# Kernel tuning notes

Hardware: AMD Instinct MI355X
Metric: run time of the kernel (lower is better)

The kernel has to match this reference:

```python
import jax, jax.numpy as jnp
import numpy as np

NEG_BIG = -9e15
LRELU_SLOPE = 0.2  # alpha

N = 8192
IN_F = 256
OUT_F = 128


def setup_inputs() -> dict:
    key = jax.random.key(0)
    k1, k2, k3, k4 = jax.random.split(key, 4)
    inputs = jax.random.normal(k1, (N, IN_F), dtype=jnp.float32)
    adj = jax.random.randint(k2, (N, N), 0, 2, dtype=jnp.int32)
    # xavier_uniform with gain=1.414
    gain = 1.414
    bW = gain * np.sqrt(6.0 / (IN_F + OUT_F))
    W = jax.random.uniform(k3, (IN_F, OUT_F), minval=-bW, maxval=bW, dtype=jnp.float32)
    ba = gain * np.sqrt(6.0 / (2 * OUT_F + 1))
    a = jax.random.uniform(k4, (2 * OUT_F, 1), minval=-ba, maxval=ba, dtype=jnp.float32)
    return {"inputs": inputs, "adj": adj, "W": W, "a": a}


def reference(inputs, adj, W, a):
    # h: [N, F']
    h = inputs @ W
    # a^T [h_i || h_j] = h_i . a[:F'] + h_j . a[F':]  -- avoids the O(N^2 * 2F') concat
    a1 = a[:OUT_F, 0]   # [F']
    a2 = a[OUT_F:, 0]   # [F']
    s1 = h @ a1         # [N]
    s2 = h @ a2         # [N]
    e = s1[:, None] + s2[None, :]                      # [N, N]
    e = jnp.where(e >= 0, e, LRELU_SLOPE * e)          # LeakyReLU(alpha)
    scores = jnp.where(adj > 0, e, jnp.float32(NEG_BIG))
    attention = jax.nn.softmax(scores, axis=1)         # row softmax; dropout p=0
    h_prime = attention @ h                            # [N, F']
    return jax.nn.elu(h_prime)                         # concat=True -> elu
```

## Files before the change

kernel.cpp:

```cpp
#include <hip/hip_runtime.h>
#include <hip/hip_bf16.h>

#define NN   8192
#define INF_ 256
#define OUTF 128
#define SLOPE 0.2f

typedef float f32x4  __attribute__((ext_vector_type(4)));
typedef float f32x16 __attribute__((ext_vector_type(16)));
typedef short bf16x8 __attribute__((ext_vector_type(8)));
typedef int   i32x4  __attribute__((ext_vector_type(4)));
typedef unsigned short u16;
typedef u16 u16x4 __attribute__((ext_vector_type(4)));

__device__ __forceinline__ u16 f2bf(float f) {
  return __builtin_bit_cast(u16, __float2bfloat16(f));
}

__global__ __launch_bounds__(256) void gat_k1(
    const float* __restrict__ X, const float* __restrict__ W,
    const float* __restrict__ a, u16* __restrict__ hbF,
    float* __restrict__ s1, float* __restrict__ s2) {
  __shared__ float xs[32 * INF_];
  const int t = threadIdx.x;
  const int r0 = blockIdx.x * 32;
  {
    const f32x4* src = (const f32x4*)(X + (size_t)r0 * INF_);
    f32x4* dst = (f32x4*)xs;
    for (int i = t; i < 32 * INF_ / 4; i += 256) dst[i] = src[i];
  }
  __syncthreads();
  const int cg = t & 31;
  const int rg = t >> 5;
  float acc[4][4];
#pragma unroll
  for (int i = 0; i < 4; i++)
#pragma unroll
    for (int j = 0; j < 4; j++) acc[i][j] = 0.f;

  for (int k = 0; k < INF_; k += 4) {
    f32x4 xv[4];
#pragma unroll
    for (int i = 0; i < 4; i++) xv[i] = *(const f32x4*)&xs[(rg * 4 + i) * INF_ + k];
#pragma unroll
    for (int kk = 0; kk < 4; kk++) {
      f32x4 wv = *(const f32x4*)&W[(k + kk) * OUTF + cg * 4];
#pragma unroll
      for (int i = 0; i < 4; i++)
#pragma unroll
        for (int j = 0; j < 4; j++) acc[i][j] = fmaf(xv[i][kk], wv[j], acc[i][j]);
    }
  }

  f32x4 a1v = *(const f32x4*)&a[cg * 4];
  f32x4 a2v = *(const f32x4*)&a[OUTF + cg * 4];
  float p1[4], p2[4];
#pragma unroll
  for (int i = 0; i < 4; i++) {
    p1[i] = acc[i][0] * a1v[0] + acc[i][1] * a1v[1] + acc[i][2] * a1v[2] + acc[i][3] * a1v[3];
    p2[i] = acc[i][0] * a2v[0] + acc[i][1] * a2v[1] + acc[i][2] * a2v[2] + acc[i][3] * a2v[3];
  }
#pragma unroll
  for (int m = 1; m < 32; m <<= 1) {
#pragma unroll
    for (int i = 0; i < 4; i++) {
      p1[i] += __shfl_xor(p1[i], m);
      p2[i] += __shfl_xor(p2[i], m);
    }
  }
  if (cg == 0) {
#pragma unroll
    for (int i = 0; i < 4; i++) {
      s1[r0 + rg * 4 + i] = p1[i];
      s2[r0 + rg * 4 + i] = p2[i];
    }
  }

  const int R0 = r0 + rg * 4;
  const int J  = R0 >> 4;
  const int gg = (R0 >> 3) & 1;
  const int e0 = R0 & 7;
#pragma unroll
  for (int j = 0; j < 4; j++) {
    const int C = cg * 4 + j;
    u16x4 pk;
#pragma unroll
    for (int i = 0; i < 4; i++) pk[i] = f2bf(acc[i][j]);
    size_t flat = ((size_t)(J * 4 + (C >> 5)) * 64 + (C & 31) + 32 * gg) * 8 + e0;
    *(u16x4*)(hbF + flat) = pk;
  }
}

__global__ __launch_bounds__(256) void gat_k2(const float* __restrict__ s2,
                                              float* __restrict__ s2m) {
  __shared__ float sm[4];
  const int t = threadIdx.x;
  float m = -1e30f;
  for (int i = t; i < NN; i += 256) m = fmaxf(m, s2[i]);
#pragma unroll
  for (int k = 1; k < 64; k <<= 1) m = fmaxf(m, __shfl_xor(m, k));
  if ((t & 63) == 0) sm[t >> 6] = m;
  __syncthreads();
  if (t == 0) *s2m = fmaxf(fmaxf(sm[0], sm[1]), fmaxf(sm[2], sm[3]));
}

__device__ __forceinline__ void st16(float* dst, const f32x16& A, int g) {
#pragma unroll
  for (int r = 0; r < 16; r++) {
    const int dr = (r & 3) + 8 * (r >> 2) + 4 * g;
    dst[dr * 128] = A[r];
  }
}
__device__ __forceinline__ void ad16(float* dst, const f32x16& A, int g) {
#pragma unroll
  for (int r = 0; r < 16; r++) {
    const int dr = (r & 3) + 8 * (r >> 2) + 4 * g;
    dst[dr * 128] += A[r];
  }
}

__global__ __launch_bounds__(512, 2) void gat_k3(
    const int* __restrict__ adj, const u16* __restrict__ hbF,
    const float* __restrict__ s1g, const float* __restrict__ s2g,
    const float* __restrict__ s2maxp, float* __restrict__ out) {
  __shared__ float lred[4 * 32 * 128];
  const int t = threadIdx.x;
  const int w = t >> 6;
  const int l = t & 63;
  const int r0 = blockIdx.x * 32;
  const int row = l & 31;
  const int g = l >> 5;

  const float s1r = s1g[r0 + row];
  const float s2m = *s2maxp;
  float Mi = s1r + s2m;
  Mi = fmaxf(Mi, SLOPE * Mi);

  f32x16 acc0 = 0.f, acc1 = 0.f, acc2 = 0.f, acc3 = 0.f;

  const i32x4* adjp = (const i32x4*)(adj + (size_t)(r0 + row) * NN + 8 * g);
  const f32x4* s2p  = (const f32x4*)(s2g + 8 * g);
  const bf16x8* bp  = (const bf16x8*)hbF;

  i32x4 a0c = adjp[4 * w], a1c = adjp[4 * w + 1];
  f32x4 s0c = s2p[4 * w],  s1c = s2p[4 * w + 1];
  bf16x8 b0c = bp[(size_t)(w * 4 + 0) * 64 + l];
  bf16x8 b1c = bp[(size_t)(w * 4 + 1) * 64 + l];
  bf16x8 b2c = bp[(size_t)(w * 4 + 2) * 64 + l];
  bf16x8 b3c = bp[(size_t)(w * 4 + 3) * 64 + l];

  float dsum = 0.f;
  for (int n = w; n < 512; n += 8) {
    const int nn = (n + 8 < 512) ? (n + 8) : w;
    i32x4 a0n = adjp[4 * nn], a1n = adjp[4 * nn + 1];
    f32x4 s0n = s2p[4 * nn],  s1n = s2p[4 * nn + 1];
    bf16x8 b0n = bp[(size_t)(nn * 4 + 0) * 64 + l];
    bf16x8 b1n = bp[(size_t)(nn * 4 + 1) * 64 + l];
    bf16x8 b2n = bp[(size_t)(nn * 4 + 2) * 64 + l];
    bf16x8 b3n = bp[(size_t)(nn * 4 + 3) * 64 + l];

    bf16x8 af;
#pragma unroll
    for (int e = 0; e < 8; e++) {
      float x = s1r + ((e < 4) ? s0c[e] : s1c[e - 4]);
      x = fmaxf(x, SLOPE * x);
      float p = __expf(x - Mi);
      const int ad = (e < 4) ? a0c[e] : a1c[e - 4];
      p = (ad > 0) ? p : 0.f;
      dsum += p;
      af[e] = (short)f2bf(p);
    }
    acc0 = __builtin_amdgcn_mfma_f32_32x32x16_bf16(af, b0c, acc0, 0, 0, 0);
    acc1 = __builtin_amdgcn_mfma_f32_32x32x16_bf16(af, b1c, acc1, 0, 0, 0);
    acc2 = __builtin_amdgcn_mfma_f32_32x32x16_bf16(af, b2c, acc2, 0, 0, 0);
    acc3 = __builtin_amdgcn_mfma_f32_32x32x16_bf16(af, b3c, acc3, 0, 0, 0);

    a0c = a0n; a1c = a1n; s0c = s0n; s1c = s1n;
    b0c = b0n; b1c = b1n; b2c = b2n; b3c = b3n;
  }

  dsum += __shfl_xor(dsum, 32);
  if (l < 32) lred[w * 32 + l] = dsum;
  __syncthreads();
  if (t < 32) {
    float d = 0.f;
#pragma unroll
    for (int w8 = 0; w8 < 8; w8++) d += lred[w8 * 32 + t];
    lred[256 + t] = d;
  }
  __syncthreads();
  const float myden = fmaxf(lred[256 + (t >> 4)], 1e-30f);
  __syncthreads();

  const int colw = l & 31;
  if (w < 4) {
    st16(&lred[w * 4096 + 0 * 32 + colw], acc0, g);
    st16(&lred[w * 4096 + 1 * 32 + colw], acc1, g);
    st16(&lred[w * 4096 + 2 * 32 + colw], acc2, g);
    st16(&lred[w * 4096 + 3 * 32 + colw], acc3, g);
  }
  __syncthreads();
  if (w >= 4) {
    ad16(&lred[(w - 4) * 4096 + 0 * 32 + colw], acc0, g);
    ad16(&lred[(w - 4) * 4096 + 1 * 32 + colw], acc1, g);
    ad16(&lred[(w - 4) * 4096 + 2 * 32 + colw], acc2, g);
    ad16(&lred[(w - 4) * 4096 + 3 * 32 + colw], acc3, g);
  }
  __syncthreads();

  const int orow = t >> 4;
  const int oc = (t & 15) * 8;
  float o[8];
#pragma unroll
  for (int i = 0; i < 8; i++) o[i] = 0.f;
#pragma unroll
  for (int b = 0; b < 4; b++)
#pragma unroll
    for (int i = 0; i < 8; i++) o[i] += lred[b * 4096 + orow * 128 + oc + i];

  float res[8];
#pragma unroll
  for (int i = 0; i < 8; i++) {
    float v = o[i] / myden;
    res[i] = (v > 0.f) ? v : expm1f(v);
  }
  float* op = out + (size_t)(r0 + orow) * OUTF + oc;
  *(f32x4*)op = (f32x4){res[0], res[1], res[2], res[3]};
  *(f32x4*)(op + 4) = (f32x4){res[4], res[5], res[6], res[7]};
}

extern "C" void kernel_launch(void* const* d_in, const int* in_sizes, int n_in,
                              void* d_out, int out_size, void* d_ws, size_t ws_size,
                              hipStream_t stream) {
  (void)in_sizes; (void)n_in; (void)out_size; (void)ws_size;
  const float* X  = (const float*)d_in[0];
  const int*  adj = (const int*)d_in[1];
  const float* W  = (const float*)d_in[2];
  const float* a  = (const float*)d_in[3];
  float* out = (float*)d_out;

  u16*   hbF = (u16*)d_ws;
  float* s1  = (float*)((char*)d_ws + (size_t)2 * 1024 * 1024);
  float* s2  = s1 + NN;
  float* s2m = s2 + NN;

  gat_k1<<<NN / 32, 256, 0, stream>>>(X, W, a, hbF, s1, s2);
  gat_k2<<<1, 256, 0, stream>>>(s2, s2m);
  gat_k3<<<NN / 32, 512, 0, stream>>>(adj, hbF, s1, s2, s2m, out);
}
```

Before: 117.2 us.

## Stage adjacency tiles through double-buffered swizzled LDS with coalesced loads

```diff
diff --git a/kernel.cpp b/kernel.cpp
--- a/kernel.cpp
+++ b/kernel.cpp
@@ -123,7 +123,7 @@
     const int* __restrict__ adj, const u16* __restrict__ hbF,
     const float* __restrict__ s1g, const float* __restrict__ s2g,
     const float* __restrict__ s2maxp, float* __restrict__ out) {
-  __shared__ float lred[4 * 32 * 128];
+  __shared__ int adjs[2 * 32 * 256];
   const int t = threadIdx.x;
   const int w = t >> 6;
   const int l = t & 63;
@@ -138,46 +138,83 @@
 
   f32x16 acc0 = 0.f, acc1 = 0.f, acc2 = 0.f, acc3 = 0.f;
 
-  const i32x4* adjp = (const i32x4*)(adj + (size_t)(r0 + row) * NN + 8 * g);
-  const f32x4* s2p  = (const f32x4*)(s2g + 8 * g);
-  const bf16x8* bp  = (const bf16x8*)hbF;
-
-  i32x4 a0c = adjp[4 * w], a1c = adjp[4 * w + 1];
-  f32x4 s0c = s2p[4 * w],  s1c = s2p[4 * w + 1];
-  bf16x8 b0c = bp[(size_t)(w * 4 + 0) * 64 + l];
-  bf16x8 b1c = bp[(size_t)(w * 4 + 1) * 64 + l];
-  bf16x8 b2c = bp[(size_t)(w * 4 + 2) * 64 + l];
-  bf16x8 b3c = bp[(size_t)(w * 4 + 3) * 64 + l];
-
+  const int srow = t >> 4;
+  const int sc4 = (t & 15) * 4;
+  const int* gsrc = adj + (size_t)(r0 + srow) * NN + sc4;
+  const int swz_s = (srow & 7) << 2;
+  const int swz_r = (row & 7) << 2;
+
+  i32x4 st[4];
+#define STAGE_LOAD(TL)                                         \
+  {                                                            \
+    const int* p_ = gsrc + 256 * (TL);                         \
+    st[0] = *(const i32x4*)(p_);                               \
+    st[1] = *(const i32x4*)(p_ + 64);                          \
+    st[2] = *(const i32x4*)(p_ + 128);                         \
+    st[3] = *(const i32x4*)(p_ + 192);                         \
+  }
+#define STAGE_WRITE(BUF)                                                    \
+  {                                                                         \
+    int* b_ = &adjs[(BUF) * 8192 + srow * 256];                             \
+    *(i32x4*)(b_ + ((sc4 + 0) ^ swz_s))   = st[0];                          \
+    *(i32x4*)(b_ + ((sc4 + 64) ^ swz_s))  = st[1];                          \
+    *(i32x4*)(b_ + ((sc4 + 128) ^ swz_s)) = st[2];                          \
+    *(i32x4*)(b_ + ((sc4 + 192) ^ swz_s)) = st[3];                          \
+  }
+
+  const bf16x8* bp = (const bf16x8*)hbF;
   float dsum = 0.f;
-  for (int n = w; n < 512; n += 8) {
-    const int nn = (n + 8 < 512) ? (n + 8) : w;
-    i32x4 a0n = adjp[4 * nn], a1n = adjp[4 * nn + 1];
-    f32x4 s0n = s2p[4 * nn],  s1n = s2p[4 * nn + 1];
-    bf16x8 b0n = bp[(size_t)(nn * 4 + 0) * 64 + l];
-    bf16x8 b1n = bp[(size_t)(nn * 4 + 1) * 64 + l];
-    bf16x8 b2n = bp[(size_t)(nn * 4 + 2) * 64 + l];
-    bf16x8 b3n = bp[(size_t)(nn * 4 + 3) * 64 + l];
-
-    bf16x8 af;
-#pragma unroll
-    for (int e = 0; e < 8; e++) {
-      float x = s1r + ((e < 4) ? s0c[e] : s1c[e - 4]);
-      x = fmaxf(x, SLOPE * x);
-      float p = __expf(x - Mi);
-      const int ad = (e < 4) ? a0c[e] : a1c[e - 4];
-      p = (ad > 0) ? p : 0.f;
-      dsum += p;
-      af[e] = (short)f2bf(p);
-    }
-    acc0 = __builtin_amdgcn_mfma_f32_32x32x16_bf16(af, b0c, acc0, 0, 0, 0);
-    acc1 = __builtin_amdgcn_mfma_f32_32x32x16_bf16(af, b1c, acc1, 0, 0, 0);
-    acc2 = __builtin_amdgcn_mfma_f32_32x32x16_bf16(af, b2c, acc2, 0, 0, 0);
-    acc3 = __builtin_amdgcn_mfma_f32_32x32x16_bf16(af, b3c, acc3, 0, 0, 0);
-
-    a0c = a0n; a1c = a1n; s0c = s0n; s1c = s1n;
-    b0c = b0n; b1c = b1n; b2c = b2n; b3c = b3n;
-  }
+
+  STAGE_LOAD(0);
+  STAGE_WRITE(0);
+  STAGE_LOAD(1);
+  __syncthreads();
+
+  int cur = 0;
+  for (int tt = 0; tt < 32; tt++) {
+    bf16x8 b[8];
+    const int n0 = 16 * tt + w;
+#pragma unroll
+    for (int k = 0; k < 2; k++) {
+      const int n = n0 + 8 * k;
+#pragma unroll
+      for (int q = 0; q < 4; q++)
+        b[k * 4 + q] = bp[(size_t)(n * 4 + q) * 64 + l];
+    }
+
+    const int* abuf = &adjs[cur * 8192 + row * 256];
+#pragma unroll
+    for (int k = 0; k < 2; k++) {
+      const int jj0 = 128 * k + 16 * w + 8 * g;
+      i32x4 A0 = *(const i32x4*)(abuf + ((jj0) ^ swz_r));
+      i32x4 A1 = *(const i32x4*)(abuf + ((jj0 + 4) ^ swz_r));
+      const int j0 = 256 * tt + jj0;
+      f32x4 s0 = *(const f32x4*)(s2g + j0);
+      f32x4 s1v = *(const f32x4*)(s2g + j0 + 4);
+      bf16x8 af;
+#pragma unroll
+      for (int e = 0; e < 8; e++) {
+        float x = s1r + ((e < 4) ? s0[e] : s1v[e - 4]);
+        x = fmaxf(x, SLOPE * x);
+        float p = __expf(x - Mi);
+        const int ad = (e < 4) ? A0[e] : A1[e - 4];
+        p = (ad > 0) ? p : 0.f;
+        dsum += p;
+        af[e] = (short)f2bf(p);
+      }
+      acc0 = __builtin_amdgcn_mfma_f32_32x32x16_bf16(af, b[k * 4 + 0], acc0, 0, 0, 0);
+      acc1 = __builtin_amdgcn_mfma_f32_32x32x16_bf16(af, b[k * 4 + 1], acc1, 0, 0, 0);
+      acc2 = __builtin_amdgcn_mfma_f32_32x32x16_bf16(af, b[k * 4 + 2], acc2, 0, 0, 0);
+      acc3 = __builtin_amdgcn_mfma_f32_32x32x16_bf16(af, b[k * 4 + 3], acc3, 0, 0, 0);
+    }
+
+    STAGE_WRITE(cur ^ 1);
+    STAGE_LOAD(tt + 2 < 32 ? tt + 2 : 0);
+    __syncthreads();
+    cur ^= 1;
+  }
+
+  float* lred = (float*)adjs;
 
   dsum += __shfl_xor(dsum, 32);
   if (l < 32) lred[w * 32 + l] = dsum;
@@ -214,9 +251,9 @@
 #pragma unroll
   for (int i = 0; i < 8; i++) o[i] = 0.f;
 #pragma unroll
-  for (int b = 0; b < 4; b++)
-#pragma unroll
-    for (int i = 0; i < 8; i++) o[i] += lred[b * 4096 + orow * 128 + oc + i];
+  for (int bq = 0; bq < 4; bq++)
+#pragma unroll
+    for (int i = 0; i < 8; i++) o[i] += lred[bq * 4096 + orow * 128 + oc + i];
 
   float res[8];
 #pragma unroll
```

Measured after the change: 116.6 us. No clear change (-0.5%).

## Split attention columns across blocks, stage adj tiles in LDS, add reduction kernel

Applied to the files above, without the earlier changes.

```diff
diff --git a/kernel.cpp b/kernel.cpp
--- a/kernel.cpp
+++ b/kernel.cpp
@@ -5,6 +5,9 @@
 #define INF_ 256
 #define OUTF 128
 #define SLOPE 0.2f
+#define NJC  4
+#define JCHUNK (NN / NJC)
+#define NT   (JCHUNK / 128)
 
 typedef float f32x4  __attribute__((ext_vector_type(4)));
 typedef float f32x16 __attribute__((ext_vector_type(16)));
@@ -119,15 +122,20 @@
   }
 }
 
-__global__ __launch_bounds__(512, 2) void gat_k3(
+__global__ __launch_bounds__(512, 4) void gat_k3(
     const int* __restrict__ adj, const u16* __restrict__ hbF,
     const float* __restrict__ s1g, const float* __restrict__ s2g,
-    const float* __restrict__ s2maxp, float* __restrict__ out) {
-  __shared__ float lred[4 * 32 * 128];
+    const float* __restrict__ s2maxp, float* __restrict__ part,
+    float* __restrict__ dpart) {
+  __shared__ int adjs[2 * 4096];
+  __shared__ float dred[256];
   const int t = threadIdx.x;
   const int w = t >> 6;
   const int l = t & 63;
-  const int r0 = blockIdx.x * 32;
+  const int rb = blockIdx.x & 255;
+  const int jc = blockIdx.x >> 8;
+  const int r0 = rb * 32;
+  const int j0 = jc * JCHUNK;
   const int row = l & 31;
   const int g = l >> 5;
 
@@ -138,95 +146,146 @@
 
   f32x16 acc0 = 0.f, acc1 = 0.f, acc2 = 0.f, acc3 = 0.f;
 
-  const i32x4* adjp = (const i32x4*)(adj + (size_t)(r0 + row) * NN + 8 * g);
-  const f32x4* s2p  = (const f32x4*)(s2g + 8 * g);
-  const bf16x8* bp  = (const bf16x8*)hbF;
-
-  i32x4 a0c = adjp[4 * w], a1c = adjp[4 * w + 1];
-  f32x4 s0c = s2p[4 * w],  s1c = s2p[4 * w + 1];
-  bf16x8 b0c = bp[(size_t)(w * 4 + 0) * 64 + l];
-  bf16x8 b1c = bp[(size_t)(w * 4 + 1) * 64 + l];
-  bf16x8 b2c = bp[(size_t)(w * 4 + 2) * 64 + l];
-  bf16x8 b3c = bp[(size_t)(w * 4 + 3) * 64 + l];
-
+  const int srow = t >> 4;
+  const int scg = t & 15;
+  const int cA = 4 * scg + ((srow & 1) ? 64 : 0);
+  const int cB = 4 * scg + ((srow & 1) ? 0 : 64);
+  const int slotA = ((cA >> 2) ^ srow) & 31;
+  const int slotB = ((cB >> 2) ^ srow) & 31;
+  const int* gsrc = adj + (size_t)(r0 + srow) * NN + j0;
+
+  i32x4 stA, stB;
+#define STAGE_LOAD(TL)                              \
+  {                                                 \
+    const int* p_ = gsrc + 128 * (TL);              \
+    stA = *(const i32x4*)(p_ + cA);                 \
+    stB = *(const i32x4*)(p_ + cB);                 \
+  }
+#define STAGE_WRITE(BUF)                            \
+  {                                                 \
+    int* b_ = &adjs[(BUF) * 4096 + srow * 128];     \
+    *(i32x4*)(b_ + slotA * 4) = stA;                \
+    *(i32x4*)(b_ + slotB * 4) = stB;                \
+  }
+
+  const int c0 = 16 * w + 8 * g;
+  const int sl0 = (((c0 >> 2) + 0) ^ row) & 31;
+  const int sl1 = (((c0 >> 2) + 1) ^ row) & 31;
+
+  const bf16x8* bp = (const bf16x8*)hbF;
+  const float* s2b = s2g + j0;
   float dsum = 0.f;
-  for (int n = w; n < 512; n += 8) {
-    const int nn = (n + 8 < 512) ? (n + 8) : w;
-    i32x4 a0n = adjp[4 * nn], a1n = adjp[4 * nn + 1];
-    f32x4 s0n = s2p[4 * nn],  s1n = s2p[4 * nn + 1];
-    bf16x8 b0n = bp[(size_t)(nn * 4 + 0) * 64 + l];
-    bf16x8 b1n = bp[(size_t)(nn * 4 + 1) * 64 + l];
-    bf16x8 b2n = bp[(size_t)(nn * 4 + 2) * 64 + l];
-    bf16x8 b3n = bp[(size_t)(nn * 4 + 3) * 64 + l];
+
+  STAGE_LOAD(0);
+  STAGE_WRITE(0);
+  STAGE_LOAD(1);
+  __syncthreads();
+
+  int cur = 0;
+  for (int tt = 0; tt < NT; tt++) {
+    const int n = jc * 128 + 8 * tt + w;
+    const bf16x8* bq = bp + (size_t)(n * 4) * 64 + l;
+    bf16x8 b0 = bq[0], b1 = bq[64], b2 = bq[128], b3 = bq[192];
+
+    const int* abuf = &adjs[cur * 4096 + row * 128];
+    i32x4 A0 = *(const i32x4*)(abuf + sl0 * 4);
+    i32x4 A1 = *(const i32x4*)(abuf + sl1 * 4);
+    f32x4 s0  = *(const f32x4*)(s2b + 128 * tt + c0);
+    f32x4 s1v = *(const f32x4*)(s2b + 128 * tt + c0 + 4);
 
     bf16x8 af;
 #pragma unroll
     for (int e = 0; e < 8; e++) {
-      float x = s1r + ((e < 4) ? s0c[e] : s1c[e - 4]);
+      float x = s1r + ((e < 4) ? s0[e] : s1v[e - 4]);
       x = fmaxf(x, SLOPE * x);
       float p = __expf(x - Mi);
-      const int ad = (e < 4) ? a0c[e] : a1c[e - 4];
+      const int ad = (e < 4) ? A0[e] : A1[e - 4];
       p = (ad > 0) ? p : 0.f;
       dsum += p;
       af[e] = (short)f2bf(p);
     }
-    acc0 = __builtin_amdgcn_mfma_f32_32x32x16_bf16(af, b0c, acc0, 0, 0, 0);
-    acc1 = __builtin_amdgcn_mfma_f32_32x32x16_bf16(af, b1c, acc1, 0, 0, 0);
-    acc2 = __builtin_amdgcn_mfma_f32_32x32x16_bf16(af, b2c, acc2, 0, 0, 0);
-    acc3 = __builtin_amdgcn_mfma_f32_32x32x16_bf16(af, b3c, acc3, 0, 0, 0);
-
-    a0c = a0n; a1c = a1n; s0c = s0n; s1c = s1n;
-    b0c = b0n; b1c = b1n; b2c = b2n; b3c = b3n;
+    acc0 = __builtin_amdgcn_mfma_f32_32x32x16_bf16(af, b0, acc0, 0, 0, 0);
+    acc1 = __builtin_amdgcn_mfma_f32_32x32x16_bf16(af, b1, acc1, 0, 0, 0);
+    acc2 = __builtin_amdgcn_mfma_f32_32x32x16_bf16(af, b2, acc2, 0, 0, 0);
+    acc3 = __builtin_amdgcn_mfma_f32_32x32x16_bf16(af, b3, acc3, 0, 0, 0);
+
+    if (tt + 1 < NT) STAGE_WRITE(cur ^ 1);
+    if (tt + 2 < NT) STAGE_LOAD(tt + 2);
+    __syncthreads();
+    cur ^= 1;
   }
 
   dsum += __shfl_xor(dsum, 32);
-  if (l < 32) lred[w * 32 + l] = dsum;
-  __syncthreads();
-  if (t < 32) {
-    float d = 0.f;
-#pragma unroll
-    for (int w8 = 0; w8 < 8; w8++) d += lred[w8 * 32 + t];
-    lred[256 + t] = d;
-  }
-  __syncthreads();
-  const float myden = fmaxf(lred[256 + (t >> 4)], 1e-30f);
-  __syncthreads();
-
+  if (l < 32) dred[w * 32 + l] = dsum;
+
+  float* lred = (float*)adjs;
   const int colw = l & 31;
-  if (w < 4) {
+  if (w < 2) {
     st16(&lred[w * 4096 + 0 * 32 + colw], acc0, g);
     st16(&lred[w * 4096 + 1 * 32 + colw], acc1, g);
     st16(&lred[w * 4096 + 2 * 32 + colw], acc2, g);
     st16(&lred[w * 4096 + 3 * 32 + colw], acc3, g);
   }
   __syncthreads();
-  if (w >= 4) {
+  if (t < 32) {
+    float d = 0.f;
+#pragma unroll
+    for (int w8 = 0; w8 < 8; w8++) d += dred[w8 * 32 + t];
+    dpart[jc * NN + r0 + t] = d;
+  }
+  if (w == 2 || w == 3) {
+    ad16(&lred[(w - 2) * 4096 + 0 * 32 + colw], acc0, g);
+    ad16(&lred[(w - 2) * 4096 + 1 * 32 + colw], acc1, g);
+    ad16(&lred[(w - 2) * 4096 + 2 * 32 + colw], acc2, g);
+    ad16(&lred[(w - 2) * 4096 + 3 * 32 + colw], acc3, g);
+  }
+  __syncthreads();
+  if (w == 4 || w == 5) {
     ad16(&lred[(w - 4) * 4096 + 0 * 32 + colw], acc0, g);
     ad16(&lred[(w - 4) * 4096 + 1 * 32 + colw], acc1, g);
     ad16(&lred[(w - 4) * 4096 + 2 * 32 + colw], acc2, g);
     ad16(&lred[(w - 4) * 4096 + 3 * 32 + colw], acc3, g);
   }
   __syncthreads();
-
-  const int orow = t >> 4;
-  const int oc = (t & 15) * 8;
-  float o[8];
-#pragma unroll
-  for (int i = 0; i < 8; i++) o[i] = 0.f;
-#pragma unroll
-  for (int b = 0; b < 4; b++)
-#pragma unroll
-    for (int i = 0; i < 8; i++) o[i] += lred[b * 4096 + orow * 128 + oc + i];
-
-  float res[8];
-#pragma unroll
-  for (int i = 0; i < 8; i++) {
-    float v = o[i] / myden;
-    res[i] = (v > 0.f) ? v : expm1f(v);
-  }
-  float* op = out + (size_t)(r0 + orow) * OUTF + oc;
-  *(f32x4*)op = (f32x4){res[0], res[1], res[2], res[3]};
-  *(f32x4*)(op + 4) = (f32x4){res[4], res[5], res[6], res[7]};
+  if (w == 6 || w == 7) {
+    ad16(&lred[(w - 6) * 4096 + 0 * 32 + colw], acc0, g);
+    ad16(&lred[(w - 6) * 4096 + 1 * 32 + colw], acc1, g);
+    ad16(&lred[(w - 6) * 4096 + 2 * 32 + colw], acc2, g);
+    ad16(&lred[(w - 6) * 4096 + 3 * 32 + colw], acc3, g);
+  }
+  __syncthreads();
+
+  const int flat = t * 8;
+  f32x4 pa = *(f32x4*)&lred[flat];
+  f32x4 pb = *(f32x4*)&lred[flat + 4];
+  pa += *(f32x4*)&lred[4096 + flat];
+  pb += *(f32x4*)&lred[4096 + flat + 4];
+  float* pp = part + (size_t)jc * (NN * OUTF) + (size_t)r0 * OUTF + flat;
+  *(f32x4*)pp = pa;
+  *(f32x4*)(pp + 4) = pb;
+}
+
+__global__ __launch_bounds__(256) void gat_k4(
+    const float* __restrict__ part, const float* __restrict__ dpart,
+    float* __restrict__ out) {
+  const int idx = blockIdx.x * 256 + threadIdx.x;
+  const int e4 = idx * 4;
+  const int i = e4 >> 7;
+  f32x4 p = {0.f, 0.f, 0.f, 0.f};
+  float d = 0.f;
+#pragma unroll
+  for (int jc = 0; jc < NJC; jc++) {
+    p += *(const f32x4*)&part[(size_t)jc * (NN * OUTF) + e4];
+    d += dpart[jc * NN + i];
+  }
+  d = fmaxf(d, 1e-30f);
+  f32x4 r;
+#pragma unroll
+  for (int k = 0; k < 4; k++) {
+    float v = p[k] / d;
+    r[k] = (v > 0.f) ? v : expm1f(v);
+  }
+  *(f32x4*)&out[e4] = r;
 }
 
 extern "C" void kernel_launch(void* const* d_in, const int* in_sizes, int n_in,
@@ -239,12 +298,16 @@
   const float* a  = (const float*)d_in[3];
   float* out = (float*)d_out;
 
-  u16*   hbF = (u16*)d_ws;
-  float* s1  = (float*)((char*)d_ws + (size_t)2 * 1024 * 1024);
-  float* s2  = s1 + NN;
-  float* s2m = s2 + NN;
+  char* ws = (char*)d_ws;
+  u16*   hbF   = (u16*)ws;
+  float* s1    = (float*)(ws + (2u << 20));
+  float* s2    = (float*)(ws + (2u << 20) + (32u << 10));
+  float* s2m   = (float*)(ws + (2u << 20) + (64u << 10));
+  float* dpart = (float*)(ws + (2u << 20) + (128u << 10));
+  float* part  = (float*)(ws + (4u << 20));
 
   gat_k1<<<NN / 32, 256, 0, stream>>>(X, W, a, hbF, s1, s2);
   gat_k2<<<1, 256, 0, stream>>>(s2, s2m);
-  gat_k3<<<NN / 32, 512, 0, stream>>>(adj, hbF, s1, s2, s2m, out);
-}
+  gat_k3<<<256 * NJC, 512, 0, stream>>>(adj, hbF, s1, s2, s2m, part, dpart);
+  gat_k4<<<(NN * OUTF / 4) / 256, 256, 0, stream>>>(part, dpart, out);
+}
```

Result: faster. 110.1 us (-6.0%).
